# Optimization experiments

Hardware: AMD Instinct MI355X
Metric: run time of the kernel (lower is better)

The kernel has to match this reference:

```python
import jax, jax.numpy as jnp
import numpy as np
import math

N_TOK = 8192; IN_DIM = 1024; D = 512; HEADS = 8; DH = D // HEADS
M = D // 2; ITERS = 6; SCALE = DH ** -0.5; KRES = 33; NCLS = 2
EPS = 1e-5


def ln(x, g, b):
    mu = jnp.mean(x, -1, keepdims=True)
    var = jnp.var(x, -1, keepdims=True)
    return (x - mu) * jax.lax.rsqrt(var + EPS) * g + b


def moore_penrose_pinv(x):
    # Newton-Schulz iterative pseudo-inverse (lucidrains nystrom-attention)
    col = jnp.abs(x).sum(-1).max()
    row = jnp.abs(x).sum(-2).max()
    z = jnp.swapaxes(x, -1, -2) / (col * row)
    I = jnp.eye(x.shape[-1], dtype=x.dtype)
    for _ in range(ITERS):
        xz = x @ z
        z = 0.25 * z @ (13 * I - xz @ (15 * I - xz @ (7 * I - xz)))
    return z


def nystrom_attn(x, qkv_w, out_w, out_b, conv_w):
    b, n, _ = x.shape
    pad = (-n) % M  # pad at FRONT so seq len divisible by num_landmarks
    xp = jnp.pad(x, ((0, 0), (pad, 0), (0, 0)))
    Np = n + pad
    q, k, v = jnp.split(xp @ qkv_w, 3, axis=-1)
    tohead = lambda t: t.reshape(b, Np, HEADS, DH).transpose(0, 2, 1, 3)  # bhnd
    q = tohead(q) * SCALE; k = tohead(k); v = tohead(v)
    l = Np // M
    q_l = q.reshape(b, HEADS, M, l, DH).mean(3)  # landmark means, bhmd
    k_l = k.reshape(b, HEADS, M, l, DH).mean(3)
    a1 = jax.nn.softmax(jnp.einsum('bhnd,bhmd->bhnm', q, k_l), -1)
    a2 = jax.nn.softmax(jnp.einsum('bhnd,bhmd->bhnm', q_l, k_l), -1)
    a3 = jax.nn.softmax(jnp.einsum('bhmd,bhnd->bhmn', q_l, k), -1)
    out = (a1 @ moore_penrose_pinv(a2)) @ (a3 @ v)
    pc = KRES // 2  # depthwise residual conv over sequence dim (groups=heads)
    out = out + jax.lax.conv_general_dilated(
        v, conv_w, (1, 1), [(pc, pc), (0, 0)],
        dimension_numbers=('NCHW', 'OIHW', 'NCHW'), feature_group_count=HEADS)
    out = out.transpose(0, 2, 1, 3).reshape(b, Np, D)
    return (out @ out_w + out_b)[:, -n:]


def ppeg(x, Hs, Ws, w7, b7, w5, b5, w3, b3):
    b, _, C = x.shape
    cls_tok, feat = x[:, :1], x[:, 1:]
    f = feat.transpose(0, 2, 1).reshape(b, C, Hs, Ws)
    def dw(w, bb, p):
        return jax.lax.conv_general_dilated(
            f, w, (1, 1), [(p, p), (p, p)],
            dimension_numbers=('NCHW', 'OIHW', 'NCHW'),
            feature_group_count=C) + bb[None, :, None, None]
    y = f + dw(w7, b7, 3) + dw(w5, b5, 2) + dw(w3, b3, 1)
    y = y.reshape(b, C, Hs * Ws).transpose(0, 2, 1)
    return jnp.concatenate([cls_tok, y], axis=1)


def setup_inputs() -> dict:
    key = jax.random.key(0)
    ks = jax.random.split(key, 16)
    s = 0.02
    return {
        'x': jax.random.normal(ks[0], (N_TOK, IN_DIM), jnp.float32),
        'fc1_w': jax.random.normal(ks[1], (IN_DIM, D), jnp.float32) * s,
        'fc1_b': jnp.zeros((D,), jnp.float32),
        'cls_token': jax.random.normal(ks[2], (1, 1, D), jnp.float32),
        'ln1_g': jnp.ones((D,), jnp.float32), 'ln1_b': jnp.zeros((D,), jnp.float32),
        'qkv1_w': jax.random.normal(ks[3], (D, 3 * D), jnp.float32) * s,
        'out1_w': jax.random.normal(ks[4], (D, D), jnp.float32) * s,
        'out1_b': jnp.zeros((D,), jnp.float32),
        'conv1_w': jax.random.normal(ks[5], (HEADS, 1, KRES, 1), jnp.float32) * s,
        'ln2_g': jnp.ones((D,), jnp.float32), 'ln2_b': jnp.zeros((D,), jnp.float32),
        'qkv2_w': jax.random.normal(ks[6], (D, 3 * D), jnp.float32) * s,
        'out2_w': jax.random.normal(ks[7], (D, D), jnp.float32) * s,
        'out2_b': jnp.zeros((D,), jnp.float32),
        'conv2_w': jax.random.normal(ks[8], (HEADS, 1, KRES, 1), jnp.float32) * s,
        'pg7_w': jax.random.normal(ks[9], (D, 1, 7, 7), jnp.float32) * s,
        'pg7_b': jnp.zeros((D,), jnp.float32),
        'pg5_w': jax.random.normal(ks[10], (D, 1, 5, 5), jnp.float32) * s,
        'pg5_b': jnp.zeros((D,), jnp.float32),
        'pg3_w': jax.random.normal(ks[11], (D, 1, 3, 3), jnp.float32) * s,
        'pg3_b': jnp.zeros((D,), jnp.float32),
        'norm_g': jnp.ones((D,), jnp.float32), 'norm_b': jnp.zeros((D,), jnp.float32),
        'fc2_w': jax.random.normal(ks[12], (D, NCLS), jnp.float32) * s,
        'fc2_b': jnp.zeros((NCLS,), jnp.float32),
    }


def reference(x, fc1_w, fc1_b, cls_token, ln1_g, ln1_b, qkv1_w, out1_w, out1_b,
              conv1_w, ln2_g, ln2_b, qkv2_w, out2_w, out2_b, conv2_w,
              pg7_w, pg7_b, pg5_w, pg5_b, pg3_w, pg3_b, norm_g, norm_b,
              fc2_w, fc2_b):
    h = jax.nn.relu(x[None].astype(jnp.float32) @ fc1_w + fc1_b)  # [1,N,D]
    n = h.shape[1]
    Hs = Ws = int(math.ceil(math.sqrt(n)))
    add = Hs * Ws - n
    h = jnp.concatenate([h, h[:, :add]], axis=1)  # pad to square by duplication
    h = jnp.concatenate([jnp.broadcast_to(cls_token, (1, 1, D)), h], axis=1)
    h = h + nystrom_attn(ln(h, ln1_g, ln1_b), qkv1_w, out1_w, out1_b, conv1_w)
    h = ppeg(h, Hs, Ws, pg7_w, pg7_b, pg5_w, pg5_b, pg3_w, pg3_b)
    h = h + nystrom_attn(ln(h, ln2_g, ln2_b), qkv2_w, out2_w, out2_b, conv2_w)
    emb = ln(h, norm_g, norm_b)[:, 0]  # cls embedding [1,D]
    logits = emb @ fc2_w + fc2_b
    Y_prob = jax.nn.softmax(logits, -1)
    Y_hat = jnp.argmax(logits, -1)
    return (logits, Y_prob, Y_hat, emb)
```

## Files before the change

### kernel.cpp

```cpp
#include <hip/hip_runtime.h>
#include <math.h>

#define NTOK   8192
#define INDIM  1024
#define NHEAD  8
#define N1     8282
#define NP     8448
#define PAD    166
#define LCH    33
#define SCALE  0.125f
#define HS     91
#define KSPLIT 24
#define KCH    (NP / KSPLIT)

typedef __attribute__((ext_vector_type(8))) _Float16 half8;
typedef __attribute__((ext_vector_type(8))) short short8;
typedef __attribute__((ext_vector_type(4))) float f32x4;
typedef unsigned short ushort_t;

#define GPTR(p) ((const __attribute__((address_space(1))) void*)(p))
#define LPTR(p) ((__attribute__((address_space(3))) void*)(p))

__device__ __forceinline__ ushort_t f2h(float f) {
    union { _Float16 h; ushort_t u; } v; v.h = (_Float16)f;
    return v.u;
}
__device__ __forceinline__ float h2f(ushort_t u) {
    union { ushort_t u; _Float16 h; } v; v.u = u;
    return (float)v.h;
}


__device__ __forceinline__ float blockReduceSumF(float v, float* red, int tid) {
    red[tid] = v; __syncthreads();
    for (int s = 128; s > 0; s >>= 1) {
        if (tid < s) red[tid] += red[tid + s];
        __syncthreads();
    }
    float r = red[0]; __syncthreads();
    return r;
}
__device__ __forceinline__ float blockReduceMaxF(float v, float* red, int tid) {
    red[tid] = v; __syncthreads();
    for (int s = 128; s > 0; s >>= 1) {
        if (tid < s) red[tid] = fmaxf(red[tid], red[tid + s]);
        __syncthreads();
    }
    float r = red[0]; __syncthreads();
    return r;
}

__global__ __launch_bounds__(256) void tcast_k(const float* __restrict__ w, ushort_t* __restrict__ wT,
                                               int K, int N)
{
    __shared__ float tb[32][33];
    int tx = threadIdx.x & 31, ty = threadIdx.x >> 5;
    int n0 = blockIdx.x * 32, k0 = blockIdx.y * 32;
#pragma unroll
    for (int i = 0; i < 4; ++i)
        tb[ty + i * 8][tx] = w[(size_t)(k0 + ty + i * 8) * N + n0 + tx];
    __syncthreads();
#pragma unroll
    for (int i = 0; i < 4; ++i)
        wT[(size_t)(n0 + ty + i * 8) * K + k0 + tx] = f2h(tb[tx][ty + i * 8]);
}

__global__ void bcast_k(const float* __restrict__ x, ushort_t* __restrict__ o)
{
    int i = blockIdx.x * 256 + threadIdx.x;
    float4 v = reinterpret_cast<const float4*>(x)[i];
    ushort4 u;
    u.x = f2h(v.x); u.y = f2h(v.y); u.z = f2h(v.z); u.w = f2h(v.w);
    reinterpret_cast<ushort4*>(o)[i] = u;
}

__global__ __launch_bounds__(256) void gemm_mn_f16(
    const ushort_t* __restrict__ A, const ushort_t* __restrict__ BT,
    const float* __restrict__ bias, const float* __restrict__ res,
    float* __restrict__ C, ushort_t* __restrict__ Ch,
    int Mvalid, int K, int lda, int ldb, int ldc, int relu, int qscale)
{
    __shared__ ushort_t As[128 * 32];
    __shared__ ushort_t Bs[64 * 32];
    const int tid = threadIdx.x;
    const int wave = tid >> 6, lane = tid & 63;
    const int row0 = blockIdx.y * 128, col0 = blockIdx.x * 64;
    const int wr = wave * 32;
    const int aRow = wave * 16 + (lane >> 2);
    const int aChS = (((lane & 3) ^ ((lane >> 3) & 3)) * 8);
    const int bRow = tid >> 2;
    const int bChS = (((tid & 3) ^ ((tid >> 3) & 3)) * 8);
    const int lr = lane & 15, lq = (lane >> 4) * 4;
    const int lks = (((lane >> 4) ^ ((lr >> 1) & 3)) * 8);
    f32x4 acc[2][4] = {};
    for (int k0 = 0; k0 < K; k0 += 32) {
        __syncthreads();
#pragma unroll
        for (int i = 0; i < 2; ++i) {
            const ushort_t* gp = A + (size_t)(row0 + i * 64 + aRow) * lda + k0 + aChS;
            __builtin_amdgcn_global_load_lds(GPTR(gp), LPTR(As + (i * 64 + wave * 16) * 32), 16, 0, 0);
        }
        const ushort_t* gq = BT + (size_t)(col0 + bRow) * ldb + k0 + bChS;
        __builtin_amdgcn_global_load_lds(GPTR(gq), LPTR(Bs + tid * 8), 16, 0, 0);
        __syncthreads();
        half8 af[2], bfr[4];
#pragma unroll
        for (int mi = 0; mi < 2; ++mi)
            af[mi] = *reinterpret_cast<const half8*>(&As[(wr + mi * 16 + lr) * 32 + lks]);
#pragma unroll
        for (int ni = 0; ni < 4; ++ni)
            bfr[ni] = *reinterpret_cast<const half8*>(&Bs[(ni * 16 + lr) * 32 + lks]);
#pragma unroll
        for (int mi = 0; mi < 2; ++mi)
#pragma unroll
            for (int ni = 0; ni < 4; ++ni)
                acc[mi][ni] = __builtin_amdgcn_mfma_f32_16x16x32_f16(af[mi], bfr[ni], acc[mi][ni], 0, 0, 0);
    }
#pragma unroll
    for (int mi = 0; mi < 2; ++mi) {
#pragma unroll
        for (int q = 0; q < 4; ++q) {
            int r = row0 + wr + mi * 16 + lq + q;
            if (r >= Mvalid) continue;
#pragma unroll
            for (int ni = 0; ni < 4; ++ni) {
                int c = col0 + ni * 16 + lr;
                float v = acc[mi][ni][q];
                if (bias) v += bias[c];
                if (res)  v += res[(size_t)r * ldc + c];
                if (relu) v = fmaxf(v, 0.f);
                if (Ch) {
                    if (qscale && c < 512) v *= SCALE;
                    Ch[(size_t)r * ldc + c] = f2h(v);
                } else {
                    C[(size_t)r * ldc + c] = v;
                }
            }
        }
    }
}

__global__ __launch_bounds__(256) void bgemm64_f16(
    const ushort_t* __restrict__ A, const ushort_t* __restrict__ B,
    ushort_t* __restrict__ C, float diag, float ss,
    ushort_t* __restrict__ C2, float diag2, float ss2)
{
    __shared__ ushort_t As[64 * 32];
    __shared__ ushort_t Bs[64 * 32];
    const int h = blockIdx.z;
    const ushort_t* Ah = A + (size_t)h * 65536;
    const ushort_t* Bh = B + (size_t)h * 65536;
    const int tid = threadIdx.x;
    const int wave = tid >> 6, lane = tid & 63;
    const int row0 = blockIdx.y * 64, col0 = blockIdx.x * 64;
    const int wr = (wave >> 1) * 32, wc = (wave & 1) * 32;
    const int aRow = tid >> 2;
    const int aChS = (((tid & 3) ^ ((tid >> 3) & 3)) * 8);
    const int kp = (tid >> 3) & 15, nc = tid & 7;
    const int kk = (kp * 2) ^ ((nc & 3) << 3);
    const int lr = lane & 15, lk = (lane >> 4) * 8, lq = (lane >> 4) * 4;
    const int lks = (((lane >> 4) ^ ((lr >> 1) & 3)) * 8);
    f32x4 acc[2][2] = {};
    for (int k0 = 0; k0 < 256; k0 += 32) {
        __syncthreads();
        const ushort_t* gp = Ah + (size_t)(row0 + aRow) * 256 + k0 + aChS;
        __builtin_amdgcn_global_load_lds(GPTR(gp), LPTR(As + tid * 8), 16, 0, 0);
        if (tid < 128) {
            const ushort_t* bp = Bh + (size_t)(k0 + kp * 2) * 256 + col0 + nc * 8;
            short8 v0 = *reinterpret_cast<const short8*>(bp);
            short8 v1 = *reinterpret_cast<const short8*>(bp + 256);
#pragma unroll
            for (int j = 0; j < 8; ++j) {
                unsigned int pk = ((unsigned int)(ushort_t)v1[j] << 16) | (unsigned int)(ushort_t)v0[j];
                *reinterpret_cast<unsigned int*>(&Bs[(nc * 8 + j) * 32 + kk]) = pk;
            }
        }
        __syncthreads();
        half8 af[2], bfr[2];
#pragma unroll
        for (int mi = 0; mi < 2; ++mi)
            af[mi] = *reinterpret_cast<const half8*>(&As[(wr + mi * 16 + lr) * 32 + lks]);
#pragma unroll
        for (int ni = 0; ni < 2; ++ni) {
            int nn = wc + ni * 16 + lr;
            bfr[ni] = *reinterpret_cast<const half8*>(&Bs[nn * 32 + (lk ^ (((nn >> 3) & 3) << 3))]);
        }
#pragma unroll
        for (int mi = 0; mi < 2; ++mi)
#pragma unroll
            for (int ni = 0; ni < 2; ++ni)
                acc[mi][ni] = __builtin_amdgcn_mfma_f32_16x16x32_f16(af[mi], bfr[ni], acc[mi][ni], 0, 0, 0);
    }
    ushort_t* Chp = C + (size_t)h * 65536;
#pragma unroll
    for (int mi = 0; mi < 2; ++mi)
#pragma unroll
        for (int ni = 0; ni < 2; ++ni)
#pragma unroll
            for (int q = 0; q < 4; ++q) {
                int r = row0 + wr + mi * 16 + lq + q;
                int c = col0 + wc + ni * 16 + lr;
                float v = ss * acc[mi][ni][q];
                if (r == c) v += diag;
                Chp[(size_t)r * 256 + c] = f2h(v);
                if (C2) {
                    float v2 = ss2 * acc[mi][ni][q];
                    if (r == c) v2 += diag2;
                    C2[(size_t)h * 65536 + (size_t)r * 256 + c] = f2h(v2);
                }
            }
}

__global__ __launch_bounds__(256) void hgemm_abT_k(
    const ushort_t* __restrict__ A, long sAh, int lda,
    const ushort_t* __restrict__ BT, long sBh, int ldb,
    ushort_t* __restrict__ C, long sCh, int ldc, int K)
{
    __shared__ ushort_t As[128 * 32];
    __shared__ ushort_t Bs[128 * 32];
    const int h = blockIdx.z;
    const ushort_t* Ah = A + (size_t)h * sAh;
    const ushort_t* Bh = BT + (size_t)h * sBh;
    ushort_t* Chp = C + (size_t)h * sCh;
    const int tid = threadIdx.x;
    const int wave = tid >> 6, lane = tid & 63;
    const int row0 = blockIdx.y * 128, col0 = blockIdx.x * 128;
    const int wr = (wave >> 1) * 64, wc = (wave & 1) * 64;
    const int sRow = wave * 16 + (lane >> 2);
    const int sChS = (((lane & 3) ^ ((lane >> 3) & 3)) * 8);
    const int lr = lane & 15, lq = (lane >> 4) * 4;
    const int lks = (((lane >> 4) ^ ((lr >> 1) & 3)) * 8);
    f32x4 acc[4][4] = {};
    for (int k0 = 0; k0 < K; k0 += 32) {
        __syncthreads();
#pragma unroll
        for (int i = 0; i < 2; ++i) {
            const ushort_t* gp = Ah + (size_t)(row0 + i * 64 + sRow) * lda + k0 + sChS;
            __builtin_amdgcn_global_load_lds(GPTR(gp), LPTR(As + (i * 64 + wave * 16) * 32), 16, 0, 0);
            const ushort_t* gq = Bh + (size_t)(col0 + i * 64 + sRow) * ldb + k0 + sChS;
            __builtin_amdgcn_global_load_lds(GPTR(gq), LPTR(Bs + (i * 64 + wave * 16) * 32), 16, 0, 0);
        }
        __syncthreads();
        half8 af[4], bfr[4];
#pragma unroll
        for (int mi = 0; mi < 4; ++mi)
            af[mi] = *reinterpret_cast<const half8*>(&As[(wr + mi * 16 + lr) * 32 + lks]);
#pragma unroll
        for (int ni = 0; ni < 4; ++ni)
            bfr[ni] = *reinterpret_cast<const half8*>(&Bs[(wc + ni * 16 + lr) * 32 + lks]);
#pragma unroll
        for (int mi = 0; mi < 4; ++mi)
#pragma unroll
            for (int ni = 0; ni < 4; ++ni)
                acc[mi][ni] = __builtin_amdgcn_mfma_f32_16x16x32_f16(af[mi], bfr[ni], acc[mi][ni], 0, 0, 0);
    }
#pragma unroll
    for (int mi = 0; mi < 4; ++mi)
#pragma unroll
        for (int q = 0; q < 4; ++q) {
            int r = row0 + wr + mi * 16 + lq + q;
#pragma unroll
            for (int ni = 0; ni < 4; ++ni)
                Chp[(size_t)r * ldc + col0 + wc + ni * 16 + lr] = f2h(acc[mi][ni][q]);
        }
}

__global__ __launch_bounds__(256) void rs3exp_k(ushort_t* __restrict__ S, float* __restrict__ rsum)
{
    __shared__ float red[256];
    int row = blockIdx.x, tid = threadIdx.x;
    ushort_t* p = S + (size_t)row * NP;
    float s = 0.f;
    for (int i = tid; i < NP; i += 256) {
        float e = __expf(h2f(p[i]));
        p[i] = f2h(e);
        s += e;
    }
    s = blockReduceSumF(s, red, tid);
    if (!tid) rsum[row] = s;
}

__global__ __launch_bounds__(256) void rs1exp_k(ushort_t* __restrict__ S, float* __restrict__ rsum)
{
    int wave = threadIdx.x >> 6, lane = threadIdx.x & 63;
    size_t row = (size_t)blockIdx.x * 4 + wave;
    ushort_t* p = S + row * 256;
    ushort4 u = *reinterpret_cast<const ushort4*>(p + lane * 4);
    float e0 = __expf(h2f(u.x)), e1 = __expf(h2f(u.y)), e2 = __expf(h2f(u.z)), e3 = __expf(h2f(u.w));
    ushort4 w;
    w.x = f2h(e0); w.y = f2h(e1); w.z = f2h(e2); w.w = f2h(e3);
    *reinterpret_cast<ushort4*>(p + lane * 4) = w;
    float s = e0 + e1 + e2 + e3;
    for (int off = 32; off; off >>= 1) s += __shfl_xor(s, off, 64);
    if (!lane) rsum[row] = s;
}

__global__ __launch_bounds__(256) void hgemm_pv_k(
    const ushort_t* __restrict__ P, const ushort_t* __restrict__ qkv16,
    float* __restrict__ part)
{
    __shared__ ushort_t As[128 * 32];
    __shared__ ushort_t Bs[64 * 32];
    const int ks = blockIdx.x, row0 = blockIdx.y * 128, h = blockIdx.z;
    const ushort_t* Ph = P + (size_t)h * 256 * NP;
    const ushort_t* V = qkv16 + 1024 + h * 64;
    const int tid = threadIdx.x;
    const int wave = tid >> 6, lane = tid & 63;
    const int wr = wave * 32;
    const int sRow = wave * 16 + (lane >> 2);
    const int sChS = (((lane & 3) ^ ((lane >> 3) & 3)) * 8);
    const int lr = lane & 15, lk = (lane >> 4) * 8, lq = (lane >> 4) * 4;
    const int lks = (((lane >> 4) ^ ((lr >> 1) & 3)) * 8);
    const int kp = (tid >> 3) & 15, nc = tid & 7;
    const int kk = (kp * 2) ^ ((nc & 3) << 3);
    f32x4 acc[2][4] = {};
    for (int k0 = ks * KCH; k0 < (ks + 1) * KCH; k0 += 32) {
        __syncthreads();
#pragma unroll
        for (int i = 0; i < 2; ++i) {
            const ushort_t* gp = Ph + (size_t)(row0 + i * 64 + sRow) * NP + k0 + sChS;
            __builtin_amdgcn_global_load_lds(GPTR(gp), LPTR(As + (i * 64 + wave * 16) * 32), 16, 0, 0);
        }
        if (tid < 128) {
            const ushort_t* bp = V + (size_t)(k0 + kp * 2) * 1536 + nc * 8;
            short8 v0 = *reinterpret_cast<const short8*>(bp);
            short8 v1 = *reinterpret_cast<const short8*>(bp + 1536);
#pragma unroll
            for (int j = 0; j < 8; ++j) {
                unsigned int pk = ((unsigned int)(ushort_t)v1[j] << 16) | (unsigned int)(ushort_t)v0[j];
                *reinterpret_cast<unsigned int*>(&Bs[(nc * 8 + j) * 32 + kk]) = pk;
            }
        }
        __syncthreads();
        half8 af[2], bfr[4];
#pragma unroll
        for (int mi = 0; mi < 2; ++mi)
            af[mi] = *reinterpret_cast<const half8*>(&As[(wr + mi * 16 + lr) * 32 + lks]);
#pragma unroll
        for (int ni = 0; ni < 4; ++ni) {
            int nn = ni * 16 + lr;
            bfr[ni] = *reinterpret_cast<const half8*>(&Bs[nn * 32 + (lk ^ (((nn >> 3) & 3) << 3))]);
        }
#pragma unroll
        for (int mi = 0; mi < 2; ++mi)
#pragma unroll
            for (int ni = 0; ni < 4; ++ni)
                acc[mi][ni] = __builtin_amdgcn_mfma_f32_16x16x32_f16(af[mi], bfr[ni], acc[mi][ni], 0, 0, 0);
    }
    float* pp = part + ((size_t)(ks * 8 + h) * 256) * 64;
#pragma unroll
    for (int mi = 0; mi < 2; ++mi)
#pragma unroll
        for (int q = 0; q < 4; ++q) {
            int r = row0 + wr + mi * 16 + lq + q;
#pragma unroll
            for (int ni = 0; ni < 4; ++ni)
                pp[(size_t)r * 64 + ni * 16 + lr] = acc[mi][ni][q];
        }
}

__global__ __launch_bounds__(256) void pv_reduce_k(const float* __restrict__ part,
                                                   const float* __restrict__ rsum,
                                                   ushort_t* __restrict__ av)
{
    int idx = blockIdx.x * 256 + threadIdx.x;
    int rc = idx >> 6;
    float s = 0.f;
#pragma unroll
    for (int ks = 0; ks < KSPLIT; ++ks)
        s += part[(size_t)ks * 131072 + idx];
    av[idx] = f2h(s / rsum[rc]);
}

__global__ void wmat_k(const ushort_t* __restrict__ z, const ushort_t* __restrict__ av,
                       ushort_t* __restrict__ W)
{
    int h = blockIdx.x >> 8, m = blockIdx.x & 255, d = threadIdx.x;
    const ushort_t* zp = z + (size_t)h * 65536 + (size_t)m * 256;
    const ushort_t* ap = av + (size_t)h * 16384 + d;
    float acc = 0.f;
    for (int j = 0; j < 256; ++j) acc += h2f(zp[j]) * h2f(ap[(size_t)j * 64]);
    W[((size_t)h * 256 + m) * 64 + d] = f2h(acc);
}

__global__ __launch_bounds__(256) void hgemm_pw_k(
    const ushort_t* __restrict__ P1, const ushort_t* __restrict__ W,
    const float* __restrict__ rsum, ushort_t* __restrict__ attn)
{
    __shared__ ushort_t As[128 * 32];
    __shared__ ushort_t Bs[64 * 32];
    const int row0 = blockIdx.y * 128, h = blockIdx.z;
    const ushort_t* Ph = P1 + (size_t)h * NP * 256;
    const ushort_t* Wh = W + (size_t)h * 16384;
    const int tid = threadIdx.x;
    const int wave = tid >> 6, lane = tid & 63;
    const int wr = wave * 32;
    const int sRow = wave * 16 + (lane >> 2);
    const int sChS = (((lane & 3) ^ ((lane >> 3) & 3)) * 8);
    const int lr = lane & 15, lk = (lane >> 4) * 8, lq = (lane >> 4) * 4;
    const int lks = (((lane >> 4) ^ ((lr >> 1) & 3)) * 8);
    const int kp = (tid >> 3) & 15, nc = tid & 7;
    const int kk = (kp * 2) ^ ((nc & 3) << 3);
    f32x4 acc[2][4] = {};
    for (int k0 = 0; k0 < 256; k0 += 32) {
        __syncthreads();
#pragma unroll
        for (int i = 0; i < 2; ++i) {
            const ushort_t* gp = Ph + (size_t)(row0 + i * 64 + sRow) * 256 + k0 + sChS;
            __builtin_amdgcn_global_load_lds(GPTR(gp), LPTR(As + (i * 64 + wave * 16) * 32), 16, 0, 0);
        }
        if (tid < 128) {
            const ushort_t* bp = Wh + (size_t)(k0 + kp * 2) * 64 + nc * 8;
            short8 v0 = *reinterpret_cast<const short8*>(bp);
            short8 v1 = *reinterpret_cast<const short8*>(bp + 64);
#pragma unroll
            for (int j = 0; j < 8; ++j) {
                unsigned int pk = ((unsigned int)(ushort_t)v1[j] << 16) | (unsigned int)(ushort_t)v0[j];
                *reinterpret_cast<unsigned int*>(&Bs[(nc * 8 + j) * 32 + kk]) = pk;
            }
        }
        __syncthreads();
        half8 af[2], bfr[4];
#pragma unroll
        for (int mi = 0; mi < 2; ++mi)
            af[mi] = *reinterpret_cast<const half8*>(&As[(wr + mi * 16 + lr) * 32 + lks]);
#pragma unroll
        for (int ni = 0; ni < 4; ++ni) {
            int nn = ni * 16 + lr;
            bfr[ni] = *reinterpret_cast<const half8*>(&Bs[nn * 32 + (lk ^ (((nn >> 3) & 3) << 3))]);
        }
#pragma unroll
        for (int mi = 0; mi < 2; ++mi)
#pragma unroll
            for (int ni = 0; ni < 4; ++ni)
                acc[mi][ni] = __builtin_amdgcn_mfma_f32_16x16x32_f16(af[mi], bfr[ni], acc[mi][ni], 0, 0, 0);
    }
#pragma unroll
    for (int mi = 0; mi < 2; ++mi)
#pragma unroll
        for (int q = 0; q < 4; ++q) {
            int t = row0 + wr + mi * 16 + lq + q;
            float inv = 1.f / rsum[(size_t)h * NP + t];
#pragma unroll
            for (int ni = 0; ni < 4; ++ni)
                attn[(size_t)t * 512 + h * 64 + ni * 16 + lr] = f2h(acc[mi][ni][q] * inv);
        }
}

__global__ void fixup_k(const float* __restrict__ cls, float* __restrict__ h)
{
    int i = blockIdx.x * 256 + threadIdx.x;
    if (i < 512) {
        h[i] = cls[i];
    } else {
        int j = i - 512;
        h[(size_t)8193 * 512 + j] = h[512 + j];
    }
}

__global__ __launch_bounds__(256) void ln_pad_k(
    const float* __restrict__ h, const float* __restrict__ g, const float* __restrict__ b,
    ushort_t* __restrict__ out)
{
    int row = blockIdx.x, tid = threadIdx.x;
    __shared__ float red[256];
    ushort_t* o = out + (size_t)row * 512;
    if (row < PAD) { o[tid] = 0; o[tid + 256] = 0; return; }
    const float* x = h + (size_t)(row - PAD) * 512;
    float v0 = x[tid], v1 = x[tid + 256];
    float mu = blockReduceSumF(v0 + v1, red, tid) * (1.f / 512.f);
    float d0 = v0 - mu, d1 = v1 - mu;
    float var = blockReduceSumF(d0 * d0 + d1 * d1, red, tid) * (1.f / 512.f);
    float rstd = rsqrtf(var + 1e-5f);
    o[tid]       = f2h(d0 * rstd * g[tid] + b[tid]);
    o[tid + 256] = f2h(d1 * rstd * g[tid + 256] + b[tid + 256]);
}

__global__ void landmark_k(const ushort_t* __restrict__ qkv, ushort_t* __restrict__ ql,
                           ushort_t* __restrict__ kl)
{
    int h = blockIdx.x >> 8, m = blockIdx.x & 255, d = threadIdx.x;
    const ushort_t* base = qkv + (size_t)(m * LCH) * 1536 + h * 64 + d;
    float sq = 0.f, sk = 0.f;
    for (int i = 0; i < LCH; ++i) {
        sq += h2f(base[(size_t)i * 1536]);
        sk += h2f(base[(size_t)i * 1536 + 512]);
    }
    ql[((size_t)h * 256 + m) * 64 + d] = f2h(sq * (1.f / (float)LCH));
    kl[((size_t)h * 256 + m) * 64 + d] = f2h(sk * (1.f / (float)LCH));
}

__global__ __launch_bounds__(256) void a2_k(
    const ushort_t* __restrict__ ql, const ushort_t* __restrict__ kl, ushort_t* __restrict__ a2)
{
    int h = blockIdx.x >> 8, r = blockIdx.x & 255, tid = threadIdx.x;
    __shared__ float qv[64]; __shared__ float red[256];
    if (tid < 64) qv[tid] = h2f(ql[((size_t)h * 256 + r) * 64 + tid]);
    __syncthreads();
    const ushort_t* kp = kl + ((size_t)h * 256 + tid) * 64;
    float dot = 0.f;
#pragma unroll
    for (int d = 0; d < 64; ++d) dot += qv[d] * h2f(kp[d]);
    float mx = blockReduceMaxF(dot, red, tid);
    float e = expf(dot - mx);
    float s = blockReduceSumF(e, red, tid);
    a2[((size_t)h * 256 + r) * 256 + tid] = f2h(e / s);
}

__global__ __launch_bounds__(256) void colsum_k(const ushort_t* __restrict__ a2, float* __restrict__ cs)
{
    int h = blockIdx.x >> 8, c = blockIdx.x & 255;
    __shared__ float red[256];
    float v = fabsf(h2f(a2[(size_t)h * 65536 + (size_t)threadIdx.x * 256 + c]));
    float s = blockReduceSumF(v, red, threadIdx.x);
    if (!threadIdx.x) cs[blockIdx.x] = s;
}
__global__ __launch_bounds__(256) void pinv_scal_k(const float* __restrict__ cs, float* __restrict__ scal)
{
    int tid = threadIdx.x; __shared__ float red[256];
    float m2 = -1e30f;
    for (int i = tid; i < 2048; i += 256) m2 = fmaxf(m2, cs[i]);
    m2 = blockReduceMaxF(m2, red, tid);
    if (!tid) scal[0] = 1.f / m2;
}
__global__ __launch_bounds__(256) void zinit_k(const ushort_t* __restrict__ a2, const float* __restrict__ scal,
                                               ushort_t* __restrict__ z)
{
    int h = blockIdx.x >> 8, r = blockIdx.x & 255, c = threadIdx.x;
    z[(size_t)h * 65536 + (size_t)r * 256 + c] =
        f2h(h2f(a2[(size_t)h * 65536 + (size_t)c * 256 + r]) * scal[0]);
}

#define CTT 64
__global__ __launch_bounds__(256) void conv2_k(const ushort_t* __restrict__ qkv,
                                               const float* __restrict__ cw,
                                               ushort_t* __restrict__ attn)
{
    __shared__ float vt[CTT + 32][64];
    int t0 = blockIdx.x * CTT;
    int h = blockIdx.y;
    int tid = threadIdx.x;
    for (int s = tid; s < (CTT + 32) * 8; s += 256) {
        int row = s >> 3, q8 = s & 7;
        int tt = t0 - 16 + row;
        if (tt >= 0 && tt < NP) {
            short8 v = *reinterpret_cast<const short8*>(qkv + (size_t)tt * 1536 + 1024 + h * 64 + q8 * 8);
#pragma unroll
            for (int j = 0; j < 8; ++j) vt[row][q8 * 8 + j] = h2f((ushort_t)v[j]);
        } else {
#pragma unroll
            for (int j = 0; j < 8; ++j) vt[row][q8 * 8 + j] = 0.f;
        }
    }
    float w33[33];
#pragma unroll
    for (int j = 0; j < 33; ++j) w33[j] = cw[h * 33 + j];
    __syncthreads();
    int c = tid & 63, tr = tid >> 6;
    float win[48];
#pragma unroll
    for (int j = 0; j < 48; ++j) win[j] = vt[tr * 16 + j][c];
#pragma unroll
    for (int i = 0; i < 16; ++i) {
        float acc = 0.f;
#pragma unroll
        for (int j = 0; j < 33; ++j) acc += w33[j] * win[i + j];
        size_t idx = (size_t)(t0 + tr * 16 + i) * 512 + h * 64 + c;
        attn[idx] = f2h(h2f(attn[idx]) + acc);
    }
}

#define PTS  16
#define PIT  22
#define PITT (PIT*PIT)
#define PCG  8
#define PSTR 12
__global__ __launch_bounds__(256) void ppeg_tiled_k(
    const float* __restrict__ hin,
    const float* __restrict__ w7, const float* __restrict__ b7,
    const float* __restrict__ w5, const float* __restrict__ b5,
    const float* __restrict__ w3, const float* __restrict__ b3,
    float* __restrict__ hout)
{
    __shared__ float inb[PITT][PSTR];
    __shared__ float wcT[49][PCG];
    __shared__ float bs[PCG];
    int tid = threadIdx.x;
    int c0 = blockIdx.z * PCG;
    int ty0 = blockIdx.y * PTS, tx0 = blockIdx.x * PTS;
    if (blockIdx.x == 0 && blockIdx.y == 0 && tid < PCG)
        hout[c0 + tid] = hin[c0 + tid];
    for (int idx = tid; idx < PITT * 2; idx += 256) {
        int tok = idx >> 1, q = idx & 1;
        int gy = ty0 - 3 + tok / PIT, gx = tx0 - 3 + tok % PIT;
        float4 v = make_float4(0.f, 0.f, 0.f, 0.f);
        if (gy >= 0 && gy < HS && gx >= 0 && gx < HS)
            v = *reinterpret_cast<const float4*>(hin + (size_t)(1 + gy * HS + gx) * 512 + c0 + q * 4);
        *reinterpret_cast<float4*>(&inb[tok][q * 4]) = v;
    }
    for (int idx = tid; idx < PCG * 49; idx += 256) {
        int c = idx / 49, t = idx % 49;
        int ky = t / 7, kx = t % 7, dy = ky - 3, dx = kx - 3;
        float w = w7[(size_t)(c0 + c) * 49 + t];
        if (dy >= -2 && dy <= 2 && dx >= -2 && dx <= 2)
            w += w5[(size_t)(c0 + c) * 25 + (dy + 2) * 5 + (dx + 2)];
        if (dy >= -1 && dy <= 1 && dx >= -1 && dx <= 1)
            w += w3[(size_t)(c0 + c) * 9 + (dy + 1) * 3 + (dx + 1)];
        wcT[t][c] = w;
    }
    if (tid < PCG) bs[tid] = b7[c0 + tid] + b5[c0 + tid] + b3[c0 + tid];
    __syncthreads();
    int oy = tid >> 4, ox = tid & 15;
    int gy = ty0 + oy, gx = tx0 + ox;
    if (gy >= HS || gx >= HS) return;
    float acc[PCG];
    {
        const float* cp = &inb[(oy + 3) * PIT + ox + 3][0];
        float4 i0 = *reinterpret_cast<const float4*>(cp);
        float4 i1 = *reinterpret_cast<const float4*>(cp + 4);
        acc[0] = i0.x + bs[0]; acc[1] = i0.y + bs[1]; acc[2] = i0.z + bs[2]; acc[3] = i0.w + bs[3];
        acc[4] = i1.x + bs[4]; acc[5] = i1.y + bs[5]; acc[6] = i1.z + bs[6]; acc[7] = i1.w + bs[7];
    }
#pragma unroll
    for (int ky = 0; ky < 7; ++ky)
#pragma unroll
        for (int kx = 0; kx < 7; ++kx) {
            int t = ky * 7 + kx;
            const float* dp = &inb[(oy + ky) * PIT + ox + kx][0];
            float4 d0 = *reinterpret_cast<const float4*>(dp);
            float4 d1 = *reinterpret_cast<const float4*>(dp + 4);
            float4 w0 = *reinterpret_cast<const float4*>(&wcT[t][0]);
            float4 w1 = *reinterpret_cast<const float4*>(&wcT[t][4]);
            acc[0] += w0.x * d0.x; acc[1] += w0.y * d0.y;
            acc[2] += w0.z * d0.z; acc[3] += w0.w * d0.w;
            acc[4] += w1.x * d1.x; acc[5] += w1.y * d1.y;
            acc[6] += w1.z * d1.z; acc[7] += w1.w * d1.w;
        }
    float* out = hout + (size_t)(1 + gy * HS + gx) * 512 + c0;
    *reinterpret_cast<float4*>(out)     = make_float4(acc[0], acc[1], acc[2], acc[3]);
    *reinterpret_cast<float4*>(out + 4) = make_float4(acc[4], acc[5], acc[6], acc[7]);
}

__global__ __launch_bounds__(256) void final_k(const float* __restrict__ h,
                                               const float* __restrict__ g, const float* __restrict__ bb,
                                               const float* __restrict__ w, const float* __restrict__ fb,
                                               float* __restrict__ out)
{
    __shared__ float red[256];
    int tid = threadIdx.x;
    float v0 = h[tid], v1 = h[tid + 256];
    float mu = blockReduceSumF(v0 + v1, red, tid) * (1.f / 512.f);
    float d0 = v0 - mu, d1 = v1 - mu;
    float var = blockReduceSumF(d0 * d0 + d1 * d1, red, tid) * (1.f / 512.f);
    float rstd = rsqrtf(var + 1e-5f);
    float e0 = d0 * rstd * g[tid] + bb[tid];
    float e1 = d1 * rstd * g[tid + 256] + bb[tid + 256];
    out[5 + tid] = e0;
    out[5 + 256 + tid] = e1;
    float l0p = e0 * w[tid * 2] + e1 * w[(tid + 256) * 2];
    float l1p = e0 * w[tid * 2 + 1] + e1 * w[(tid + 256) * 2 + 1];
    float l0 = blockReduceSumF(l0p, red, tid);
    float l1 = blockReduceSumF(l1p, red, tid);
    if (!tid) {
        l0 += fb[0]; l1 += fb[1];
        out[0] = l0; out[1] = l1;
        float mx = fmaxf(l0, l1);
        float p0 = expf(l0 - mx), p1 = expf(l1 - mx);
        float si = 1.f / (p0 + p1);
        out[2] = p0 * si; out[3] = p1 * si;
        out[4] = (l1 > l0) ? 1.f : 0.f;
    }
}

struct WsPtrs {
    float *h, *h2, *cs, *scal, *rsum3, *rsum1, *part;
    ushort_t *xbB, *qkv16, *ql16, *kl16, *a2h, *zh, *z2h, *xzh, *t1h, *t2h;
    ushort_t *av16, *W16, *qkvT, *outT, *x16, *fc1T, *S16;
};

static void run_attn(float* hbuf, const float* ln_g, const float* ln_b,
                     const float* qkv_w, const float* out_w, const float* out_b,
                     const float* conv_w, const WsPtrs& P, hipStream_t s)
{
    tcast_k<<<dim3(1536 / 32, 512 / 32), 256, 0, s>>>(qkv_w, P.qkvT, 512, 1536);
    tcast_k<<<dim3(512 / 32, 512 / 32), 256, 0, s>>>(out_w, P.outT, 512, 512);
    ln_pad_k<<<NP, 256, 0, s>>>(hbuf, ln_g, ln_b, P.xbB);
    gemm_mn_f16<<<dim3(1536 / 64, NP / 128), 256, 0, s>>>(P.xbB, P.qkvT, nullptr, nullptr,
                                                          nullptr, P.qkv16, NP, 512, 512, 512, 1536, 0, 1);
    landmark_k<<<2048, 64, 0, s>>>(P.qkv16, P.ql16, P.kl16);
    a2_k<<<2048, 256, 0, s>>>(P.ql16, P.kl16, P.a2h);
    colsum_k<<<2048, 256, 0, s>>>(P.a2h, P.cs);
    pinv_scal_k<<<1, 256, 0, s>>>(P.cs, P.scal);
    zinit_k<<<2048, 256, 0, s>>>(P.a2h, P.scal, P.zh);
    ushort_t* za = P.zh; ushort_t* zb = P.z2h;
    for (int it = 0; it < 6; ++it) {
        bgemm64_f16<<<dim3(4, 4, 8), 256, 0, s>>>(P.a2h, za, P.xzh, 0.f, 1.f, P.t1h, 7.f, -1.f);
        bgemm64_f16<<<dim3(4, 4, 8), 256, 0, s>>>(P.xzh, P.t1h, P.t2h, 15.f, -1.f, nullptr, 0.f, 0.f);
        bgemm64_f16<<<dim3(4, 4, 8), 256, 0, s>>>(P.xzh, P.t2h, P.t1h, 13.f, -1.f, nullptr, 0.f, 0.f);
        bgemm64_f16<<<dim3(4, 4, 8), 256, 0, s>>>(za, P.t1h, zb, 0.f, 0.25f, nullptr, 0.f, 0.f);
        ushort_t* tmp = za; za = zb; zb = tmp;
    }
    hgemm_abT_k<<<dim3(NP / 128, 2, 8), 256, 0, s>>>(P.ql16, 16384, 64,
                                                     P.qkv16 + 512, 64, 1536,
                                                     P.S16, (long)256 * NP, NP, 64);
    rs3exp_k<<<2048, 256, 0, s>>>(P.S16, P.rsum3);
    hgemm_pv_k<<<dim3(KSPLIT, 2, 8), 256, 0, s>>>(P.S16, P.qkv16, P.part);
    pv_reduce_k<<<512, 256, 0, s>>>(P.part, P.rsum3, P.av16);
    wmat_k<<<2048, 64, 0, s>>>(za, P.av16, P.W16);
    hgemm_abT_k<<<dim3(2, NP / 128, 8), 256, 0, s>>>(P.qkv16, 64, 1536,
                                                     P.kl16, 16384, 64,
                                                     P.S16, (long)NP * 256, 256, 64);
    rs1exp_k<<<(8 * NP) / 4, 256, 0, s>>>(P.S16, P.rsum1);
    hgemm_pw_k<<<dim3(1, NP / 128, 8), 256, 0, s>>>(P.S16, P.W16, P.rsum1, P.xbB);
    conv2_k<<<dim3(NP / CTT, 8), 256, 0, s>>>(P.qkv16, conv_w, P.xbB);
    gemm_mn_f16<<<dim3(512 / 64, (N1 + 127) / 128), 256, 0, s>>>(P.xbB + (size_t)PAD * 512, P.outT,
                                                                 out_b, hbuf, hbuf, nullptr,
                                                                 N1, 512, 512, 512, 512, 0, 0);
}

extern "C" void kernel_launch(void* const* d_in, const int* in_sizes, int n_in,
                              void* d_out, int out_size, void* d_ws, size_t ws_size,
                              hipStream_t stream)
{
    (void)in_sizes; (void)n_in; (void)out_size; (void)ws_size;
    const float* x       = (const float*)d_in[0];
    const float* fc1_w   = (const float*)d_in[1];
    const float* fc1_b   = (const float*)d_in[2];
    const float* cls_tok = (const float*)d_in[3];
    const float* ln1_g   = (const float*)d_in[4];
    const float* ln1_b   = (const float*)d_in[5];
    const float* qkv1_w  = (const float*)d_in[6];
    const float* out1_w  = (const float*)d_in[7];
    const float* out1_b  = (const float*)d_in[8];
    const float* conv1_w = (const float*)d_in[9];
    const float* ln2_g   = (const float*)d_in[10];
    const float* ln2_b   = (const float*)d_in[11];
    const float* qkv2_w  = (const float*)d_in[12];
    const float* out2_w  = (const float*)d_in[13];
    const float* out2_b  = (const float*)d_in[14];
    const float* conv2_w = (const float*)d_in[15];
    const float* pg7_w   = (const float*)d_in[16];
    const float* pg7_b   = (const float*)d_in[17];
    const float* pg5_w   = (const float*)d_in[18];
    const float* pg5_b   = (const float*)d_in[19];
    const float* pg3_w   = (const float*)d_in[20];
    const float* pg3_b   = (const float*)d_in[21];
    const float* norm_g  = (const float*)d_in[22];
    const float* norm_b  = (const float*)d_in[23];
    const float* fc2_w   = (const float*)d_in[24];
    const float* fc2_b   = (const float*)d_in[25];

    float* ws = (float*)d_ws;
    WsPtrs P;
    float* cur = ws;
    P.h     = cur; cur += (size_t)N1 * 512;
    P.h2    = cur; cur += (size_t)N1 * 512;
    P.xbB   = (ushort_t*)cur; cur += (size_t)NP * 512 / 2;
    P.qkv16 = (ushort_t*)cur; cur += (size_t)NP * 1536 / 2;
    P.ql16  = (ushort_t*)cur; cur += 65536;
    P.kl16  = (ushort_t*)cur; cur += 65536;
    P.a2h   = (ushort_t*)cur; cur += 262144;
    P.zh    = (ushort_t*)cur; cur += 262144;
    P.z2h   = (ushort_t*)cur; cur += 262144;
    P.xzh   = (ushort_t*)cur; cur += 262144;
    P.t1h   = (ushort_t*)cur; cur += 262144;
    P.t2h   = (ushort_t*)cur; cur += 262144;
    P.av16  = (ushort_t*)cur; cur += 65536;
    P.W16   = (ushort_t*)cur; cur += 65536;
    P.cs    = cur; cur += 2048;
    P.scal  = cur; cur += 64;
    P.qkvT  = (ushort_t*)cur; cur += 393216 + 64;
    P.outT  = (ushort_t*)cur; cur += 131072 + 64;
    P.rsum3 = cur; cur += 2048;
    P.rsum1 = cur; cur += (size_t)8 * NP;
    P.part  = cur; cur += (size_t)KSPLIT * 131072;
    P.S16   = (ushort_t*)cur; cur += (size_t)8 * 256 * NP / 2;
    P.x16   = P.S16;
    P.fc1T  = P.S16 + (size_t)NTOK * INDIM;

    bcast_k<<<(NTOK * INDIM) / 1024, 256, 0, stream>>>(x, P.x16);
    tcast_k<<<dim3(512 / 32, 1024 / 32), 256, 0, stream>>>(fc1_w, P.fc1T, 1024, 512);
    gemm_mn_f16<<<dim3(512 / 64, NTOK / 128), 256, 0, stream>>>(P.x16, P.fc1T, fc1_b, nullptr,
                                                                P.h + 512, nullptr,
                                                                NTOK, 1024, 1024, 1024, 512, 1, 0);
    fixup_k<<<180, 256, 0, stream>>>(cls_tok, P.h);
    run_attn(P.h, ln1_g, ln1_b, qkv1_w, out1_w, out1_b, conv1_w, P, stream);
    ppeg_tiled_k<<<dim3(6, 6, 512 / PCG), 256, 0, stream>>>(P.h, pg7_w, pg7_b, pg5_w, pg5_b,
                                                            pg3_w, pg3_b, P.h2);
    run_attn(P.h2, ln2_g, ln2_b, qkv2_w, out2_w, out2_b, conv2_w, P, stream);
    final_k<<<1, 256, 0, stream>>>(P.h2, norm_g, norm_b, fc2_w, fc2_b, (float*)d_out);
}
```

Before: 798.1 us.

## Fuse exp and row-sum into score GEMM epilogue; widen landmark/wmat blocks

The exp and row-sum softmax steps, which were separate kernels re-reading and rewriting the large fp16 score matrices, now run in the hgemm_abT epilogue. Each wave shuffle-reduces its row partial sums and adds them to rsum with atomicAdd. A single zero_k launch clears the accumulators, which assumes rsum1 sits right after rsum3 in the workspace. landmark_k and wmat_k now pack four 64-thread rows into each 256-thread block, so there are fewer tiny blocks. The cost is atomic contention on the row sums and a dependence on workspace layout.

Result: no change. 792.7 us (-0.7%).

```diff
diff --git a/kernel.cpp b/kernel.cpp
--- a/kernel.cpp
+++ b/kernel.cpp
@@ -48,6 +48,12 @@
     }
     float r = red[0]; __syncthreads();
     return r;
+}
+
+__global__ void zero_k(float* __restrict__ p)
+{
+    int i = blockIdx.x * 256 + threadIdx.x;
+    reinterpret_cast<float4*>(p)[i] = make_float4(0.f, 0.f, 0.f, 0.f);
 }
 
 __global__ __launch_bounds__(256) void tcast_k(const float* __restrict__ w, ushort_t* __restrict__ wT,
@@ -214,7 +220,8 @@
 __global__ __launch_bounds__(256) void hgemm_abT_k(
     const ushort_t* __restrict__ A, long sAh, int lda,
     const ushort_t* __restrict__ BT, long sBh, int ldb,
-    ushort_t* __restrict__ C, long sCh, int ldc, int K)
+    ushort_t* __restrict__ C, long sCh, int ldc, int K,
+    float* __restrict__ rsum, int sRsum)
 {
     __shared__ ushort_t As[128 * 32];
     __shared__ ushort_t Bs[128 * 32];
@@ -259,40 +266,16 @@
 #pragma unroll
         for (int q = 0; q < 4; ++q) {
             int r = row0 + wr + mi * 16 + lq + q;
-#pragma unroll
-            for (int ni = 0; ni < 4; ++ni)
-                Chp[(size_t)r * ldc + col0 + wc + ni * 16 + lr] = f2h(acc[mi][ni][q]);
-        }
-}
-
-__global__ __launch_bounds__(256) void rs3exp_k(ushort_t* __restrict__ S, float* __restrict__ rsum)
-{
-    __shared__ float red[256];
-    int row = blockIdx.x, tid = threadIdx.x;
-    ushort_t* p = S + (size_t)row * NP;
-    float s = 0.f;
-    for (int i = tid; i < NP; i += 256) {
-        float e = __expf(h2f(p[i]));
-        p[i] = f2h(e);
-        s += e;
-    }
-    s = blockReduceSumF(s, red, tid);
-    if (!tid) rsum[row] = s;
-}
-
-__global__ __launch_bounds__(256) void rs1exp_k(ushort_t* __restrict__ S, float* __restrict__ rsum)
-{
-    int wave = threadIdx.x >> 6, lane = threadIdx.x & 63;
-    size_t row = (size_t)blockIdx.x * 4 + wave;
-    ushort_t* p = S + row * 256;
-    ushort4 u = *reinterpret_cast<const ushort4*>(p + lane * 4);
-    float e0 = __expf(h2f(u.x)), e1 = __expf(h2f(u.y)), e2 = __expf(h2f(u.z)), e3 = __expf(h2f(u.w));
-    ushort4 w;
-    w.x = f2h(e0); w.y = f2h(e1); w.z = f2h(e2); w.w = f2h(e3);
-    *reinterpret_cast<ushort4*>(p + lane * 4) = w;
-    float s = e0 + e1 + e2 + e3;
-    for (int off = 32; off; off >>= 1) s += __shfl_xor(s, off, 64);
-    if (!lane) rsum[row] = s;
+            float s = 0.f;
+#pragma unroll
+            for (int ni = 0; ni < 4; ++ni) {
+                float e = __expf(acc[mi][ni][q]);
+                Chp[(size_t)r * ldc + col0 + wc + ni * 16 + lr] = f2h(e);
+                s += e;
+            }
+            for (int off = 8; off; off >>= 1) s += __shfl_xor(s, off, 64);
+            if (lr == 0) atomicAdd(&rsum[(size_t)h * sRsum + r], s);
+        }
 }
 
 __global__ __launch_bounds__(256) void hgemm_pv_k(
@@ -372,10 +355,12 @@
     av[idx] = f2h(s / rsum[rc]);
 }
 
-__global__ void wmat_k(const ushort_t* __restrict__ z, const ushort_t* __restrict__ av,
-                       ushort_t* __restrict__ W)
-{
-    int h = blockIdx.x >> 8, m = blockIdx.x & 255, d = threadIdx.x;
+__global__ __launch_bounds__(256) void wmat_k(const ushort_t* __restrict__ z,
+                                              const ushort_t* __restrict__ av,
+                                              ushort_t* __restrict__ W)
+{
+    int idx = blockIdx.x * 4 + (threadIdx.x >> 6);
+    int h = idx >> 8, m = idx & 255, d = threadIdx.x & 63;
     const ushort_t* zp = z + (size_t)h * 65536 + (size_t)m * 256;
     const ushort_t* ap = av + (size_t)h * 16384 + d;
     float acc = 0.f;
@@ -476,10 +461,12 @@
     o[tid + 256] = f2h(d1 * rstd * g[tid + 256] + b[tid + 256]);
 }
 
-__global__ void landmark_k(const ushort_t* __restrict__ qkv, ushort_t* __restrict__ ql,
-                           ushort_t* __restrict__ kl)
-{
-    int h = blockIdx.x >> 8, m = blockIdx.x & 255, d = threadIdx.x;
+__global__ __launch_bounds__(256) void landmark_k(const ushort_t* __restrict__ qkv,
+                                                  ushort_t* __restrict__ ql,
+                                                  ushort_t* __restrict__ kl)
+{
+    int idx = blockIdx.x * 4 + (threadIdx.x >> 6);
+    int h = idx >> 8, m = idx & 255, d = threadIdx.x & 63;
     const ushort_t* base = qkv + (size_t)(m * LCH) * 1536 + h * 64 + d;
     float sq = 0.f, sk = 0.f;
     for (int i = 0; i < LCH; ++i) {
@@ -687,7 +674,7 @@
     ln_pad_k<<<NP, 256, 0, s>>>(hbuf, ln_g, ln_b, P.xbB);
     gemm_mn_f16<<<dim3(1536 / 64, NP / 128), 256, 0, s>>>(P.xbB, P.qkvT, nullptr, nullptr,
                                                           nullptr, P.qkv16, NP, 512, 512, 512, 1536, 0, 1);
-    landmark_k<<<2048, 64, 0, s>>>(P.qkv16, P.ql16, P.kl16);
+    landmark_k<<<512, 256, 0, s>>>(P.qkv16, P.ql16, P.kl16);
     a2_k<<<2048, 256, 0, s>>>(P.ql16, P.kl16, P.a2h);
     colsum_k<<<2048, 256, 0, s>>>(P.a2h, P.cs);
     pinv_scal_k<<<1, 256, 0, s>>>(P.cs, P.scal);
@@ -700,17 +687,18 @@
         bgemm64_f16<<<dim3(4, 4, 8), 256, 0, s>>>(za, P.t1h, zb, 0.f, 0.25f, nullptr, 0.f, 0.f);
         ushort_t* tmp = za; za = zb; zb = tmp;
     }
+    zero_k<<<68, 256, 0, s>>>(P.rsum3);
     hgemm_abT_k<<<dim3(NP / 128, 2, 8), 256, 0, s>>>(P.ql16, 16384, 64,
                                                      P.qkv16 + 512, 64, 1536,
-                                                     P.S16, (long)256 * NP, NP, 64);
-    rs3exp_k<<<2048, 256, 0, s>>>(P.S16, P.rsum3);
+                                                     P.S16, (long)256 * NP, NP, 64,
+                                                     P.rsum3, 256);
     hgemm_pv_k<<<dim3(KSPLIT, 2, 8), 256, 0, s>>>(P.S16, P.qkv16, P.part);
     pv_reduce_k<<<512, 256, 0, s>>>(P.part, P.rsum3, P.av16);
-    wmat_k<<<2048, 64, 0, s>>>(za, P.av16, P.W16);
+    wmat_k<<<512, 256, 0, s>>>(za, P.av16, P.W16);
     hgemm_abT_k<<<dim3(2, NP / 128, 8), 256, 0, s>>>(P.qkv16, 64, 1536,
                                                      P.kl16, 16384, 64,
-                                                     P.S16, (long)NP * 256, 256, 64);
-    rs1exp_k<<<(8 * NP) / 4, 256, 0, s>>>(P.S16, P.rsum1);
+                                                     P.S16, (long)NP * 256, 256, 64,
+                                                     P.rsum1, NP);
     hgemm_pw_k<<<dim3(1, NP / 128, 8), 256, 0, s>>>(P.S16, P.W16, P.rsum1, P.xbB);
     conv2_k<<<dim3(NP / CTT, 8), 256, 0, s>>>(P.qkv16, conv_w, P.xbB);
     gemm_mn_f16<<<dim3(512 / 64, (N1 + 127) / 128), 256, 0, s>>>(P.xbB + (size_t)PAD * 512, P.outT,
```
